# Optimization experiments

Measured on AMD Instinct MI355X. Metric: run time of the kernel, lower is better.

## Reference

```python
import jax, jax.numpy as jnp
import numpy as np

TEMPERATURE = 0.1
B, S, D, V = 4, 256, 768, 50257


def setup_inputs() -> dict:
    key = jax.random.key(0)
    k1, k2 = jax.random.split(key)
    return {
        "pred_embeds": jax.random.normal(k1, (B, S, D), dtype=jnp.float32),
        "embed_weight": jax.random.normal(k2, (V, D), dtype=jnp.float32),
    }


def reference(pred_embeds, embed_weight):
    # metric == 'l2': scores = -||p - t||^2, computed via the GEMM identity
    # -(||p||^2 + ||t||^2 - 2 p.t) instead of a (B,S,V,D) broadcast diff.
    p_sq = jnp.sum(pred_embeds * pred_embeds, axis=-1)        # (B,S)
    t_sq = jnp.sum(embed_weight * embed_weight, axis=-1)      # (V,)
    dot = jnp.einsum('bsd,vd->bsv', pred_embeds, embed_weight)  # (B,S,V)
    scores = 2.0 * dot - p_sq[..., None] - t_sq               # (B,S,V)

    softmax_pred_probs = jax.nn.softmax(scores / TEMPERATURE, axis=-1)
    predictions = jnp.argmax(softmax_pred_probs, axis=-1)      # (B,S) int

    # straight-through one-hot over probs
    y_hard = jax.nn.one_hot(predictions, V, dtype=softmax_pred_probs.dtype)
    pred_probs = y_hard - jax.lax.stop_gradient(softmax_pred_probs) + softmax_pred_probs

    # straight-through embedding lookup
    n_pred_embs = embed_weight[predictions]                    # (B,S,D)
    pred_embeds_st = pred_embeds + jax.lax.stop_gradient(n_pred_embs - pred_embeds)

    return (pred_embeds_st, pred_embeds, predictions, pred_probs, softmax_pred_probs)
```

## Files before the change

### kernel.cpp

```cpp
#include <hip/hip_runtime.h>
#include <math.h>

namespace {

constexpr int Bb = 4, Ss = 256, Dd = 768, Vv = 50257;
constexpr int Mm = Bb * Ss;
constexpr int BM = 128, BN = 128, BK = 32;
constexpr int NS = Dd / BK;
constexpr int TW = (Vv + BN - 1) / BN;
constexpr int TA = Mm / BM;
constexpr int NT2 = TW * 2;
constexpr int CHUNK = BM * BK;
constexpr float SC = 14.4269504088896341f;

constexpr int PSTRIDE = 17;
constexpr int PCOUNT  = 128 * 2 * PSTRIDE;
constexpr size_t SMEM_BYTES = (size_t)PCOUNT * 4 * 3;

typedef _Float16 f16x8 __attribute__((ext_vector_type(8)));
typedef float f32x4 __attribute__((ext_vector_type(4)));

constexpr size_t WPLANE = (size_t)TW * NS * CHUNK;
constexpr size_t APLANE = (size_t)TA * NS * CHUNK;

__device__ __forceinline__ void gload_lds16(const void* g, void* l) {
    typedef __attribute__((address_space(3))) void lds_t;
    typedef const __attribute__((address_space(1))) void gm_t;
    __builtin_amdgcn_global_load_lds((gm_t*)g, (lds_t*)l, 16, 0, 0);
}

__global__ __launch_bounds__(256) void convert_pack_tsq(const float* __restrict__ src,
                                                        _Float16* __restrict__ hp,
                                                        _Float16* __restrict__ lp,
                                                        float* __restrict__ sumsq,
                                                        int nrows) {
    const int t   = blockIdx.x;
    const int tid = threadIdx.x;
    const int r   = blockIdx.y * 64 + (tid >> 2);
    const int q   = tid & 3;
    const int v   = t * BM + r;
    const bool valid = v < nrows;

    float sq = 0.f;
#pragma unroll
    for (int i = 0; i < 6; ++i) {
        const int s = q * 6 + i;
        float vals[32];
        if (valid) {
            const float4* p = reinterpret_cast<const float4*>(src + (size_t)v * Dd + s * BK);
#pragma unroll
            for (int k = 0; k < 8; ++k) *reinterpret_cast<float4*>(&vals[4 * k]) = p[k];
        } else {
#pragma unroll
            for (int k = 0; k < 32; ++k) vals[k] = 0.f;
        }
        const size_t chunk = ((size_t)t * NS + s) * CHUNK;
#pragma unroll
        for (int fq = 0; fq < 4; ++fq) {
            _Float16 hi[8], lo[8];
#pragma unroll
            for (int e = 0; e < 8; ++e) {
                const float x = vals[fq * 8 + e];
                sq = fmaf(x, x, sq);
                const _Float16 h = (_Float16)x;
                hi[e] = h;
                lo[e] = (_Float16)(x - (float)h);
            }
            *reinterpret_cast<f16x8*>(&hp[chunk + fq * (BM * 8) + (size_t)r * 8]) =
                *reinterpret_cast<const f16x8*>(hi);
            *reinterpret_cast<f16x8*>(&lp[chunk + fq * (BM * 8) + (size_t)r * 8]) =
                *reinterpret_cast<const f16x8*>(lo);
        }
    }
    sq += __shfl_xor(sq, 1);
    sq += __shfl_xor(sq, 2);
    if (valid && q == 0) sumsq[v] = sq;
}

__global__ __launch_bounds__(256) void gemm_kernel(const _Float16* __restrict__ Ahp,
                                                   const _Float16* __restrict__ Alp,
                                                   const _Float16* __restrict__ Whp,
                                                   const _Float16* __restrict__ Wlp,
                                                   const float* __restrict__ tsq,
                                                   float* __restrict__ scores,
                                                   float* __restrict__ pmax,
                                                   int*   __restrict__ pidx,
                                                   float* __restrict__ psum) {
    __shared__ __align__(16) char smem_raw[SMEM_BYTES];
    _Float16 (*lds)[CHUNK] = reinterpret_cast<_Float16(*)[CHUNK]>(smem_raw);

    const int b    = blockIdx.x;
    const int xcd  = b & 7;
    const int slot = b >> 3;
    const int tn   = xcd * 50 + (slot >> 3);
    const int tm   = slot & 7;
    if (tn >= TW) return;

    const int tid  = threadIdx.x;
    const int wid  = tid >> 6;
    const int lane = tid & 63;
    const int wr   = wid >> 1;
    const int wc   = wid & 1;
    const int fr   = lane & 15;
    const int fq   = lane >> 4;

    const _Float16* gA_h = Ahp + (size_t)tm * NS * CHUNK;
    const _Float16* gA_l = Alp + (size_t)tm * NS * CHUNK;
    const _Float16* gW_h = Whp + (size_t)tn * NS * CHUNK;
    const _Float16* gW_l = Wlp + (size_t)tn * NS * CHUNK;

    f32x4 acc[4][4];
#pragma unroll
    for (int m = 0; m < 4; ++m)
#pragma unroll
        for (int n = 0; n < 4; ++n) acc[m][n] = (f32x4){0.f, 0.f, 0.f, 0.f};

    for (int s = 0; s < NS; ++s) {
        if (s) __syncthreads();
        const size_t so = (size_t)s * CHUNK;
        const _Float16* gsrc[4] = {gA_h + so, gA_l + so, gW_h + so, gW_l + so};
#pragma unroll
        for (int c = 0; c < 4; ++c) {
#pragma unroll
            for (int i = 0; i < 2; ++i) {
                const int seg = wid * 2 + i;
                gload_lds16(gsrc[c] + seg * 512 + lane * 8, &lds[c][seg * 512]);
            }
        }
        __syncthreads();

        f16x8 ah[4], al[4];
#pragma unroll
        for (int m = 0; m < 4; ++m) {
            const int r = wr * 64 + m * 16 + fr;
            ah[m] = *reinterpret_cast<const f16x8*>(&lds[0][fq * (BM * 8) + r * 8]);
            al[m] = *reinterpret_cast<const f16x8*>(&lds[1][fq * (BM * 8) + r * 8]);
        }
#pragma unroll
        for (int n = 0; n < 4; ++n) {
            const int c = wc * 64 + n * 16 + fr;
            const f16x8 wh = *reinterpret_cast<const f16x8*>(&lds[2][fq * (BM * 8) + c * 8]);
            const f16x8 wl = *reinterpret_cast<const f16x8*>(&lds[3][fq * (BM * 8) + c * 8]);
#pragma unroll
            for (int m = 0; m < 4; ++m) {
                acc[m][n] = __builtin_amdgcn_mfma_f32_16x16x32_f16(ah[m], wh, acc[m][n], 0, 0, 0);
                acc[m][n] = __builtin_amdgcn_mfma_f32_16x16x32_f16(al[m], wh, acc[m][n], 0, 0, 0);
                acc[m][n] = __builtin_amdgcn_mfma_f32_16x16x32_f16(ah[m], wl, acc[m][n], 0, 0, 0);
            }
        }
    }

    __syncthreads();
    float* pmL = reinterpret_cast<float*>(smem_raw);
    float* psL = pmL + PCOUNT;
    int*   piL = reinterpret_cast<int*>(psL + PCOUNT);

    float tq[4];
    int   gcol[4];
    bool  ok[4];
#pragma unroll
    for (int n = 0; n < 4; ++n) {
        gcol[n] = tn * BN + wc * 64 + n * 16 + fr;
        ok[n]   = gcol[n] < Vv;
        tq[n]   = ok[n] ? tsq[gcol[n]] : 0.f;
    }

#pragma unroll
    for (int m = 0; m < 4; ++m) {
#pragma unroll
        for (int r = 0; r < 4; ++r) {
            const int rloc = wr * 64 + m * 16 + fq * 4 + r;
            const int grow = tm * BM + rloc;
            float vmax = -INFINITY;
            int   vidx = 0x7fffffff;
#pragma unroll
            for (int n = 0; n < 4; ++n) {
                if (ok[n]) {
                    const float sv = fmaf(2.f, acc[m][n][r], -tq[n]);
                    scores[(size_t)grow * Vv + gcol[n]] = sv;
                    if (sv > vmax) { vmax = sv; vidx = gcol[n]; }
                }
            }
            float ls = 0.f;
#pragma unroll
            for (int n = 0; n < 4; ++n) {
                if (ok[n]) {
                    const float sv = fmaf(2.f, acc[m][n][r], -tq[n]);
                    ls += exp2f((sv - vmax) * SC);
                }
            }
            const int o = (rloc * 2 + wc) * PSTRIDE + fr;
            pmL[o] = vmax;
            psL[o] = ls;
            piL[o] = vidx;
        }
    }
    __syncthreads();

    {
        const int rloc = tid >> 1;
        const int wcs  = tid & 1;
        float m = -INFINITY, s = 0.f;
        int   id = 0x7fffffff;
#pragma unroll
        for (int f = 0; f < 16; ++f) {
            const int o = (rloc * 2 + wcs) * PSTRIDE + f;
            const float m2 = pmL[o];
            const int   i2 = piL[o];
            const float s2 = psL[o];
            if (m2 > m || (m2 == m && i2 < id)) {
                s = ((m > -INFINITY) ? s * exp2f((m - m2) * SC) : 0.f) + s2;
                m = m2; id = i2;
            } else {
                s += s2 * exp2f((m2 - m) * SC);
            }
        }
        const int grow = tm * BM + rloc;
        const int cidx = tn * 2 + wcs;
        const size_t o = (size_t)grow * NT2 + cidx;
        pmax[o] = m;
        pidx[o] = id;
        psum[o] = s;
    }
}

__global__ __launch_bounds__(256) void reduce_stats(const float* __restrict__ pmax,
                                                    const int*   __restrict__ pidx,
                                                    const float* __restrict__ psum,
                                                    float* __restrict__ out1,
                                                    float* __restrict__ out2) {
    const int row = blockIdx.x;
    const int tid = threadIdx.x;
    const size_t base = (size_t)row * NT2;

    float m = -INFINITY, s = 0.f;
    int   id = 0x7fffffff;
    for (int c = tid; c < NT2; c += 256) {
        const float m2 = pmax[base + c];
        const int   i2 = pidx[base + c];
        const float s2 = psum[base + c];
        if (m2 > m || (m2 == m && i2 < id)) {
            s = ((m > -INFINITY) ? s * exp2f((m - m2) * SC) : 0.f) + s2;
            m = m2; id = i2;
        } else {
            s += (m2 > -INFINITY) ? s2 * exp2f((m2 - m) * SC) : 0.f;
        }
    }

    __shared__ float smax[256];
    __shared__ int   sidx[256];
    __shared__ float ssum[256];
    smax[tid] = m; sidx[tid] = id; ssum[tid] = s;
    __syncthreads();
#pragma unroll
    for (int off = 128; off > 0; off >>= 1) {
        if (tid < off) {
            const float m1 = smax[tid], m2 = smax[tid + off];
            const int   i1 = sidx[tid], i2 = sidx[tid + off];
            const float s1 = ssum[tid], s2 = ssum[tid + off];
            if (m2 > m1 || (m2 == m1 && i2 < i1)) {
                smax[tid] = m2; sidx[tid] = i2;
                ssum[tid] = ((m1 > -INFINITY) ? s1 * exp2f((m1 - m2) * SC) : 0.f) + s2;
            } else {
                ssum[tid] = s1 + ((m2 > -INFINITY) ? s2 * exp2f((m2 - m1) * SC) : 0.f);
            }
        }
        __syncthreads();
    }
    if (tid == 0) {
        out2[row] = (float)sidx[0];
        out1[(size_t)row * Dd + 766] = smax[0];
        out1[(size_t)row * Dd + 767] = 1.0f / ssum[0];
    }
}

__global__ __launch_bounds__(256) void finalize_kernel(const float* __restrict__ A,
                                                       const float* __restrict__ W,
                                                       float* __restrict__ out0,
                                                       float* __restrict__ out1,
                                                       float* __restrict__ out2,
                                                       float* __restrict__ out3,
                                                       float* __restrict__ out4) {
    const int row = blockIdx.x;
    const int tid = threadIdx.x;
    float* srow = out4 + (size_t)row * Vv;
    float* hrow = out3 + (size_t)row * Vv;
    constexpr int NV4 = Vv >> 2;

    const float gmax = out1[(size_t)row * Dd + 766];
    const float inv  = out1[(size_t)row * Dd + 767];
    const int   pred = (int)out2[row];

    const float4* s4 = reinterpret_cast<const float4*>(srow);
    float4* p4 = reinterpret_cast<float4*>(srow);
    float4* h4 = reinterpret_cast<float4*>(hrow);
    for (int i = tid; i < NV4; i += 256) {
        const float4 v = s4[i];
        const int b = 4 * i;
        float4 p, h;
        p.x = exp2f((v.x - gmax) * SC) * inv;
        p.y = exp2f((v.y - gmax) * SC) * inv;
        p.z = exp2f((v.z - gmax) * SC) * inv;
        p.w = exp2f((v.w - gmax) * SC) * inv;
        h.x = (b + 0 == pred) ? 1.f : 0.f;
        h.y = (b + 1 == pred) ? 1.f : 0.f;
        h.z = (b + 2 == pred) ? 1.f : 0.f;
        h.w = (b + 3 == pred) ? 1.f : 0.f;
        p4[i] = p;
        h4[i] = h;
    }
    if (tid == 0) {
        const float val = srow[Vv - 1];
        srow[Vv - 1] = exp2f((val - gmax) * SC) * inv;
        hrow[Vv - 1] = (pred == Vv - 1) ? 1.f : 0.f;
    }

    __syncthreads();

    const float4* wrow = reinterpret_cast<const float4*>(W + (size_t)pred * Dd);
    const float4* arow = reinterpret_cast<const float4*>(A + (size_t)row * Dd);
    float4* o0 = reinterpret_cast<float4*>(out0 + (size_t)row * Dd);
    float4* o1 = reinterpret_cast<float4*>(out1 + (size_t)row * Dd);
    if (tid < Dd / 4) {
        o0[tid] = wrow[tid];
        o1[tid] = arow[tid];
    }
}

}

extern "C" void kernel_launch(void* const* d_in, const int* in_sizes, int n_in,
                              void* d_out, int out_size, void* d_ws, size_t ws_size,
                              hipStream_t stream) {
    const float* pred_embeds  = (const float*)d_in[0];
    const float* embed_weight = (const float*)d_in[1];

    float* out  = (float*)d_out;
    float* out0 = out;
    float* out1 = out0 + (size_t)Mm * Dd;
    float* out2 = out1 + (size_t)Mm * Dd;
    float* out3 = out2 + Mm;
    float* out4 = out3 + (size_t)Mm * Vv;

    _Float16* Whp = (_Float16*)out3;
    _Float16* Wlp = Whp + WPLANE;
    _Float16* Ahp = Wlp + WPLANE;
    _Float16* Alp = Ahp + APLANE;
    float*    tsq = (float*)(Alp + APLANE);
    float*    asq = tsq + Vv;
    float*    pmax = asq + Mm;
    int*      pidx = (int*)(pmax + (size_t)Mm * NT2);
    float*    psum = (float*)(pidx + (size_t)Mm * NT2);

    convert_pack_tsq<<<dim3(TW, 2), 256, 0, stream>>>(embed_weight, Whp, Wlp, tsq, Vv);
    convert_pack_tsq<<<dim3(TA, 2), 256, 0, stream>>>(pred_embeds, Ahp, Alp, asq, Mm);

    gemm_kernel<<<3200, 256, 0, stream>>>(Ahp, Alp, Whp, Wlp, tsq, out4,
                                          pmax, pidx, psum);

    reduce_stats<<<Mm, 256, 0, stream>>>(pmax, pidx, psum, out1, out2);

    finalize_kernel<<<Mm, 256, 0, stream>>>(pred_embeds, embed_weight,
                                            out0, out1, out2, out3, out4);
}
```

Measured before the change: 501.5 us.

## Replace LDS epilogue reduction with shuffle-based partial stats and remap convert threads

```diff
diff --git a/kernel.cpp b/kernel.cpp
--- a/kernel.cpp
+++ b/kernel.cpp
@@ -9,13 +9,9 @@
 constexpr int NS = Dd / BK;
 constexpr int TW = (Vv + BN - 1) / BN;
 constexpr int TA = Mm / BM;
-constexpr int NT2 = TW * 2;
+constexpr int NT8 = TW * 8;
 constexpr int CHUNK = BM * BK;
 constexpr float SC = 14.4269504088896341f;
-
-constexpr int PSTRIDE = 17;
-constexpr int PCOUNT  = 128 * 2 * PSTRIDE;
-constexpr size_t SMEM_BYTES = (size_t)PCOUNT * 4 * 3;
 
 typedef _Float16 f16x8 __attribute__((ext_vector_type(8)));
 typedef float f32x4 __attribute__((ext_vector_type(4)));
@@ -34,17 +30,21 @@
                                                         _Float16* __restrict__ lp,
                                                         float* __restrict__ sumsq,
                                                         int nrows) {
-    const int t   = blockIdx.x;
-    const int tid = threadIdx.x;
-    const int r   = blockIdx.y * 64 + (tid >> 2);
-    const int q   = tid & 3;
-    const int v   = t * BM + r;
+    const int t    = blockIdx.x;
+    const int tid  = threadIdx.x;
+    const int wid  = tid >> 6;
+    const int lane = tid & 63;
+    const int r    = (wid & 1) * 64 + lane;
+    const int s0   = blockIdx.y * 12 + (wid >> 1) * 6;
+    const int v    = t * BM + r;
     const bool valid = v < nrows;
 
+    __shared__ float sq_lds[2][128];
+
     float sq = 0.f;
 #pragma unroll
     for (int i = 0; i < 6; ++i) {
-        const int s = q * 6 + i;
+        const int s = s0 + i;
         float vals[32];
         if (valid) {
             const float4* p = reinterpret_cast<const float4*>(src + (size_t)v * Dd + s * BK);
@@ -57,24 +57,27 @@
         const size_t chunk = ((size_t)t * NS + s) * CHUNK;
 #pragma unroll
         for (int fq = 0; fq < 4; ++fq) {
-            _Float16 hi[8], lo[8];
+            _Float16 hi8[8], lo8[8];
 #pragma unroll
             for (int e = 0; e < 8; ++e) {
                 const float x = vals[fq * 8 + e];
                 sq = fmaf(x, x, sq);
                 const _Float16 h = (_Float16)x;
-                hi[e] = h;
-                lo[e] = (_Float16)(x - (float)h);
+                hi8[e] = h;
+                lo8[e] = (_Float16)(x - (float)h);
             }
             *reinterpret_cast<f16x8*>(&hp[chunk + fq * (BM * 8) + (size_t)r * 8]) =
-                *reinterpret_cast<const f16x8*>(hi);
+                *reinterpret_cast<const f16x8*>(hi8);
             *reinterpret_cast<f16x8*>(&lp[chunk + fq * (BM * 8) + (size_t)r * 8]) =
-                *reinterpret_cast<const f16x8*>(lo);
-        }
-    }
-    sq += __shfl_xor(sq, 1);
-    sq += __shfl_xor(sq, 2);
-    if (valid && q == 0) sumsq[v] = sq;
+                *reinterpret_cast<const f16x8*>(lo8);
+        }
+    }
+    sq_lds[wid >> 1][r] = sq;
+    __syncthreads();
+    if (tid < 128) {
+        const int vv = t * BM + tid;
+        if (vv < nrows) atomicAdd(&sumsq[vv], sq_lds[0][tid] + sq_lds[1][tid]);
+    }
 }
 
 __global__ __launch_bounds__(256) void gemm_kernel(const _Float16* __restrict__ Ahp,
@@ -86,8 +89,7 @@
                                                    float* __restrict__ pmax,
                                                    int*   __restrict__ pidx,
                                                    float* __restrict__ psum) {
-    __shared__ __align__(16) char smem_raw[SMEM_BYTES];
-    _Float16 (*lds)[CHUNK] = reinterpret_cast<_Float16(*)[CHUNK]>(smem_raw);
+    __shared__ _Float16 lds[4][CHUNK];
 
     const int b    = blockIdx.x;
     const int xcd  = b & 7;
@@ -150,11 +152,6 @@
         }
     }
 
-    __syncthreads();
-    float* pmL = reinterpret_cast<float*>(smem_raw);
-    float* psL = pmL + PCOUNT;
-    int*   piL = reinterpret_cast<int*>(psL + PCOUNT);
-
     float tq[4];
     int   gcol[4];
     bool  ok[4];
@@ -171,56 +168,43 @@
         for (int r = 0; r < 4; ++r) {
             const int rloc = wr * 64 + m * 16 + fq * 4 + r;
             const int grow = tm * BM + rloc;
+            float sv[4];
             float vmax = -INFINITY;
             int   vidx = 0x7fffffff;
 #pragma unroll
             for (int n = 0; n < 4; ++n) {
+                sv[n] = ok[n] ? fmaf(2.f, acc[m][n][r], -tq[n]) : -INFINITY;
                 if (ok[n]) {
-                    const float sv = fmaf(2.f, acc[m][n][r], -tq[n]);
-                    scores[(size_t)grow * Vv + gcol[n]] = sv;
-                    if (sv > vmax) { vmax = sv; vidx = gcol[n]; }
+                    scores[(size_t)grow * Vv + gcol[n]] = sv[n];
+                    if (sv[n] > vmax) { vmax = sv[n]; vidx = gcol[n]; }
                 }
             }
             float ls = 0.f;
-#pragma unroll
-            for (int n = 0; n < 4; ++n) {
-                if (ok[n]) {
-                    const float sv = fmaf(2.f, acc[m][n][r], -tq[n]);
-                    ls += exp2f((sv - vmax) * SC);
+            if (vmax > -INFINITY) {
+#pragma unroll
+                for (int n = 0; n < 4; ++n)
+                    if (ok[n]) ls += exp2f((sv[n] - vmax) * SC);
+            }
+#pragma unroll
+            for (int off = 1; off <= 2; off <<= 1) {
+                const float om = __shfl_xor(vmax, off);
+                const int   oi = __shfl_xor(vidx, off);
+                const float os = __shfl_xor(ls,  off);
+                if (om > vmax || (om == vmax && om > -INFINITY && oi < vidx)) {
+                    ls = ((vmax > -INFINITY) ? ls * exp2f((vmax - om) * SC) : 0.f) + os;
+                    vmax = om; vidx = oi;
+                } else if (om > -INFINITY) {
+                    ls += os * exp2f((om - vmax) * SC);
                 }
             }
-            const int o = (rloc * 2 + wc) * PSTRIDE + fr;
-            pmL[o] = vmax;
-            psL[o] = ls;
-            piL[o] = vidx;
-        }
-    }
-    __syncthreads();
-
-    {
-        const int rloc = tid >> 1;
-        const int wcs  = tid & 1;
-        float m = -INFINITY, s = 0.f;
-        int   id = 0x7fffffff;
-#pragma unroll
-        for (int f = 0; f < 16; ++f) {
-            const int o = (rloc * 2 + wcs) * PSTRIDE + f;
-            const float m2 = pmL[o];
-            const int   i2 = piL[o];
-            const float s2 = psL[o];
-            if (m2 > m || (m2 == m && i2 < id)) {
-                s = ((m > -INFINITY) ? s * exp2f((m - m2) * SC) : 0.f) + s2;
-                m = m2; id = i2;
-            } else {
-                s += s2 * exp2f((m2 - m) * SC);
-            }
-        }
-        const int grow = tm * BM + rloc;
-        const int cidx = tn * 2 + wcs;
-        const size_t o = (size_t)grow * NT2 + cidx;
-        pmax[o] = m;
-        pidx[o] = id;
-        psum[o] = s;
+            if ((fr & 3) == 0) {
+                const int cidx = (tn * 2 + wc) * 4 + (fr >> 2);
+                const size_t o = (size_t)grow * NT8 + cidx;
+                pmax[o] = vmax;
+                pidx[o] = vidx;
+                psum[o] = ls;
+            }
+        }
     }
 }
 
@@ -231,19 +215,19 @@
                                                     float* __restrict__ out2) {
     const int row = blockIdx.x;
     const int tid = threadIdx.x;
-    const size_t base = (size_t)row * NT2;
+    const size_t base = (size_t)row * NT8;
 
     float m = -INFINITY, s = 0.f;
     int   id = 0x7fffffff;
-    for (int c = tid; c < NT2; c += 256) {
+    for (int c = tid; c < NT8; c += 256) {
         const float m2 = pmax[base + c];
         const int   i2 = pidx[base + c];
         const float s2 = psum[base + c];
-        if (m2 > m || (m2 == m && i2 < id)) {
+        if (m2 > m || (m2 == m && m2 > -INFINITY && i2 < id)) {
             s = ((m > -INFINITY) ? s * exp2f((m - m2) * SC) : 0.f) + s2;
             m = m2; id = i2;
-        } else {
-            s += (m2 > -INFINITY) ? s2 * exp2f((m2 - m) * SC) : 0.f;
+        } else if (m2 > -INFINITY) {
+            s += s2 * exp2f((m2 - m) * SC);
         }
     }
 
@@ -258,11 +242,11 @@
             const float m1 = smax[tid], m2 = smax[tid + off];
             const int   i1 = sidx[tid], i2 = sidx[tid + off];
             const float s1 = ssum[tid], s2 = ssum[tid + off];
-            if (m2 > m1 || (m2 == m1 && i2 < i1)) {
+            if (m2 > m1 || (m2 == m1 && m2 > -INFINITY && i2 < i1)) {
                 smax[tid] = m2; sidx[tid] = i2;
                 ssum[tid] = ((m1 > -INFINITY) ? s1 * exp2f((m1 - m2) * SC) : 0.f) + s2;
-            } else {
-                ssum[tid] = s1 + ((m2 > -INFINITY) ? s2 * exp2f((m2 - m1) * SC) : 0.f);
+            } else if (m2 > -INFINITY) {
+                ssum[tid] = s1 + s2 * exp2f((m2 - m1) * SC);
             }
         }
         __syncthreads();
@@ -349,8 +333,10 @@
     float*    tsq = (float*)(Alp + APLANE);
     float*    asq = tsq + Vv;
     float*    pmax = asq + Mm;
-    int*      pidx = (int*)(pmax + (size_t)Mm * NT2);
-    float*    psum = (float*)(pidx + (size_t)Mm * NT2);
+    int*      pidx = (int*)(pmax + (size_t)Mm * NT8);
+    float*    psum = (float*)(pidx + (size_t)Mm * NT8);
+
+    hipMemsetAsync(tsq, 0, (size_t)(Vv + Mm) * sizeof(float), stream);
 
     convert_pack_tsq<<<dim3(TW, 2), 256, 0, stream>>>(embed_weight, Whp, Wlp, tsq, Vv);
     convert_pack_tsq<<<dim3(TA, 2), 256, 0, stream>>>(pred_embeds, Ahp, Alp, asq, Mm);
```

Result: slower. 538.2 us (+7.3%).
